# Kernel optimization log

Hardware: AMD Instinct MI355X
Metric: run time of the kernel (lower is better)

The kernel has to match this reference:

```python
import jax, jax.numpy as jnp
import numpy as np

S, B, D = 2048, 2, 1024
NH, DH, DI = 16, 64, 4096


def setup_inputs() -> dict:
    key = jax.random.key(0)
    ks = jax.random.split(key, 12)
    init_qkv = 1.0 / np.sqrt(D)
    init_out = 1.0 / np.sqrt(NH * DH)
    stdm = 1.0 / np.sqrt(D)
    stdi = 1.0 / np.sqrt(DI)

    def u(k, shape, lo, hi):
        return jax.random.uniform(k, shape, jnp.float32, lo, hi)

    inp = {}
    inp["dec_inp"] = jax.random.normal(ks[0], (S, B, D), jnp.float32)
    # causal mask: True = masked (future key j > query i); shape [q, k, batch]
    causal = jnp.triu(jnp.ones((S, S), bool), k=1)
    inp["attn_mask"] = jnp.broadcast_to(causal[:, :, None], (S, S, B))
    inp["query_mean"] = u(ks[1], (NH * DH, D), -init_qkv, init_qkv)
    inp["key_mean"] = u(ks[2], (NH * DH, D), -init_qkv, init_qkv)
    inp["value_mean"] = u(ks[3], (NH * DH, D), -init_qkv, init_qkv)
    inp["query_std"] = u(ks[4], (NH * DH, D), 2 * np.log(init_qkv), np.log(init_qkv))
    inp["key_std"] = u(ks[5], (NH * DH, D), 2 * np.log(init_qkv), np.log(init_qkv))
    inp["value_std"] = u(ks[6], (NH * DH, D), 2 * np.log(init_qkv), np.log(init_qkv))
    inp["output_mean"] = u(ks[7], (D, NH * DH), -init_out, init_out)
    inp["output_std"] = u(ks[8], (D, NH * DH), 2 * np.log(init_out), np.log(init_out))
    inp["ln1_gamma"] = jnp.ones((D,), jnp.float32)
    inp["ln1_beta"] = jnp.zeros((D,), jnp.float32)
    inp["w1_mean"] = u(ks[9], (DI, D), -stdm, stdm)
    inp["w2_mean"] = u(ks[10], (D, DI), -stdi, stdi)
    inp["w1_std"] = u(ks[11], (DI, D), 2 * np.log(stdm), np.log(stdm))
    inp["w2_std"] = u(jax.random.fold_in(key, 99), (D, DI), 2 * np.log(stdi), np.log(stdi))
    inp["ln2_gamma"] = jnp.ones((D,), jnp.float32)
    inp["ln2_beta"] = jnp.zeros((D,), jnp.float32)
    return inp


def _layer_norm(x, g, b, eps=1e-5):
    mu = jnp.mean(x, -1, keepdims=True)
    var = jnp.mean((x - mu) ** 2, -1, keepdims=True)
    return g * (x - mu) * jax.lax.rsqrt(var + eps) + b


def _kl(theta_mean, theta_std):
    return jnp.mean(theta_mean ** 2 - 2.0 * theta_std + jnp.exp(2.0 * theta_std)) / 2.0


def reference(dec_inp, attn_mask, query_mean, key_mean, value_mean, query_std,
              key_std, value_std, output_mean, output_std, ln1_gamma, ln1_beta,
              w1_mean, w2_mean, w1_std, w2_std, ln2_gamma, ln2_beta):
    scale = 1.0 / (DH ** 0.5)
    # QKV projections (eval mode: no Bayesian weight sampling, diffs are 0)
    head_q = jnp.einsum('ibd,hd->ibh', dec_inp, query_mean).reshape(S, B, NH, DH)
    head_k = jnp.einsum('ibd,hd->ibh', dec_inp, key_mean).reshape(S, B, NH, DH)
    head_v = jnp.einsum('ibd,hd->ibh', dec_inp, value_mean).reshape(S, B, NH, DH)
    attn_score = jnp.einsum('ibnd,jbnd->ijbn', head_q, head_k) * scale
    attn_score = jnp.where(attn_mask[:, :, :, None], -jnp.inf, attn_score)
    attn_prob = jax.nn.softmax(attn_score, axis=1)  # softmax over key dim j
    attn_vec = jnp.einsum('ijbn,jbnd->ibnd', attn_prob, head_v).reshape(S, B, NH * DH)
    # NOTE: the original code (bug-faithfully) projects with value_mean, not output_mean
    attn_out = jnp.einsum('ibh,dh->ibd', attn_vec, value_mean)
    h = _layer_norm(dec_inp + attn_out, ln1_gamma, ln1_beta)
    attn_kl = _kl(
        jnp.concatenate([query_mean, key_mean, value_mean, output_mean.T], -1),
        jnp.concatenate([query_std, key_std, value_std, output_std.T], -1))
    # Bayesian positionwise FF (no activation in BayesPositionwiseFF)
    l1 = jnp.einsum('ibd,fd->ibf', h, w1_mean)
    l2 = jnp.einsum('ibf,df->ibd', l1, w2_mean)
    out = _layer_norm(h + l2, ln2_gamma, ln2_beta)
    ff_kl = _kl(jnp.concatenate([w1_mean, w2_mean.T], -1),
                jnp.concatenate([w1_std, w2_std.T], -1))
    return out, attn_kl + ff_kl
```

## Files before the change

### kernel.cpp

```cpp
#include <hip/hip_runtime.h>

#define S_LEN  2048
#define BATCH  2
#define DMODEL 1024
#define NHEADS 16
#define DHEAD  64
#define DFF    4096
#define MROWS  (S_LEN*BATCH)
#define QKVN   3072

typedef __attribute__((ext_vector_type(8))) short bf16x8;
typedef __attribute__((ext_vector_type(4))) float f32x4;
typedef __attribute__((ext_vector_type(4))) short s16x4;

#define NEG_BIG (-3.0e38f)
#define SCALE_LOG2 (0.125f * 1.4426950408889634f)

__device__ __forceinline__ short f2bf(float f){
  unsigned u = __float_as_uint(f);
  u += 0x7fffu + ((u >> 16) & 1u);
  return (short)(u >> 16);
}

__device__ __forceinline__ void gload16(const void* gptr, void* lptr){
  __builtin_amdgcn_global_load_lds(
      (const __attribute__((address_space(1))) unsigned int*)gptr,
      (__attribute__((address_space(3))) unsigned int*)lptr,
      16, 0, 0);
}

__global__ __launch_bounds__(256) void cast_kernel(const float* __restrict__ in,
                                                   short* __restrict__ out, int n){
  int i = (blockIdx.x * 256 + threadIdx.x) * 4;
  if (i >= n) return;
  f32x4 v = *(const f32x4*)(in + i);
  s16x4 o;
  o[0] = f2bf(v[0]); o[1] = f2bf(v[1]); o[2] = f2bf(v[2]); o[3] = f2bf(v[3]);
  *(s16x4*)(out + i) = o;
}

__global__ __launch_bounds__(256) void cast_kl_kernel(const float* __restrict__ mean,
                                                      const float* __restrict__ stdv,
                                                      short* __restrict__ outb,
                                                      int n, double* acc){
  __shared__ double red[4];
  double local = 0.0;
  const int stride = gridDim.x * 1024;
  for (int i = (blockIdx.x * 256 + threadIdx.x) * 4; i < n; i += stride){
    f32x4 m = *(const f32x4*)(mean + i);
    f32x4 sv = *(const f32x4*)(stdv + i);
    if (outb){
      s16x4 o;
      o[0] = f2bf(m[0]); o[1] = f2bf(m[1]); o[2] = f2bf(m[2]); o[3] = f2bf(m[3]);
      *(s16x4*)(outb + i) = o;
    }
    for (int e = 0; e < 4; e++)
      local += (double)(m[e] * m[e]) - 2.0 * (double)sv[e] + (double)expf(2.f * sv[e]);
  }
  for (int msk = 1; msk < 64; msk <<= 1) local += __shfl_xor(local, msk, 64);
  const int t = threadIdx.x;
  if ((t & 63) == 0) red[t >> 6] = local;
  __syncthreads();
  if (t == 0) atomicAdd(acc, red[0] + red[1] + red[2] + red[3]);
}

__global__ void kl_final(const double* acc, float* out){
  out[0] = (float)(acc[0] / 8388608.0 + acc[1] / 16777216.0);
}

template<int BN>
__global__ __launch_bounds__(512) void gemm_bt(const short* __restrict__ A,
                                               const short* __restrict__ Bt,
                                               float* __restrict__ Cf,
                                               short* __restrict__ Cb,
                                               int M, int N, int K, int nbx){
  __shared__ short As[3][128][32];
  __shared__ short Bs[3][BN][32];
  constexpr int NB = BN / 32;
  constexpr int BSTRIDE = BN * 64;
  const int t = threadIdx.x;
  const int lane = t & 63, w = t >> 6;
  const int q8 = (int)gridDim.x >> 3;
  const int sid = ((int)blockIdx.x & 7) * q8 + ((int)blockIdx.x >> 3);
  const int bx = sid % nbx, by = sid / nbx;
  const int m0 = by * 128, n0 = bx * BN;
  const int wm = (w & 3) * 32, wn = (w >> 2) * (BN / 2);
  const int lr = lane & 15, lg = lane >> 4;
  const bool doB = (BN == 128) || (t < 256);

  f32x4 acc[2][NB] = {};

  const short* Ap = A  + (size_t)(m0 + (t >> 2)) * K + (t & 3) * 8;
  const short* Bp = Bt + (size_t)(n0 + ((t & (BN * 4 - 1)) >> 2)) * K + (t & 3) * 8;
  char* ldsA0 = (char*)As + w * 1024;
  char* ldsB0 = (char*)Bs + (w & (NB * 2 - 1)) * 1024;

  const int nk = K / 32;
  for (int p = 0; p < 2; p++){
    gload16(Ap + p * 32, ldsA0 + p * 8192);
    if (doB) gload16(Bp + p * 32, ldsB0 + p * BSTRIDE);
  }

  int bufcur = 0;
  for (int kt = 0; kt < nk; kt++){
    if (kt + 1 < nk){
      if (doB) asm volatile("s_waitcnt vmcnt(2)" ::: "memory");
      else     asm volatile("s_waitcnt vmcnt(1)" ::: "memory");
    } else {
      asm volatile("s_waitcnt vmcnt(0)" ::: "memory");
    }
    __builtin_amdgcn_s_barrier();
    asm volatile("" ::: "memory");

    if (kt + 2 < nk){
      int bnx = bufcur >= 1 ? bufcur - 1 : bufcur + 2;
      gload16(Ap + (kt + 2) * 32, ldsA0 + bnx * 8192);
      if (doB) gload16(Bp + (kt + 2) * 32, ldsB0 + bnx * BSTRIDE);
    }

    bf16x8 a0 = *(const bf16x8*)&As[bufcur][wm      + lr][lg * 8];
    bf16x8 a1 = *(const bf16x8*)&As[bufcur][wm + 16 + lr][lg * 8];
    bf16x8 bfr[NB];
    for (int ni = 0; ni < NB; ni++)
      bfr[ni] = *(const bf16x8*)&Bs[bufcur][wn + ni * 16 + lr][lg * 8];
    __builtin_amdgcn_s_setprio(1);
    for (int ni = 0; ni < NB; ni++){
      acc[0][ni] = __builtin_amdgcn_mfma_f32_16x16x32_bf16(a0, bfr[ni], acc[0][ni], 0, 0, 0);
      acc[1][ni] = __builtin_amdgcn_mfma_f32_16x16x32_bf16(a1, bfr[ni], acc[1][ni], 0, 0, 0);
    }
    __builtin_amdgcn_s_setprio(0);
    bufcur = bufcur < 2 ? bufcur + 1 : 0;
  }

  for (int mi = 0; mi < 2; mi++){
    for (int ni = 0; ni < NB; ni++){
      int row = m0 + wm + mi * 16 + lg * 4;
      int col = n0 + wn + ni * 16 + lr;
      for (int r = 0; r < 4; r++){
        float v = acc[mi][ni][r];
        if (Cf) Cf[(size_t)(row + r) * N + col] = v;
        if (Cb) Cb[(size_t)(row + r) * N + col] = f2bf(v);
      }
    }
  }
}

__global__ __launch_bounds__(256) void attn_kernel(const short* __restrict__ QKV,
                                                   short* __restrict__ AV){
  __shared__ short Ks[64][64];
  __shared__ short Vst[64][64];
  __shared__ short Pt[4][16][64];
  const int t = threadIdx.x, lane = t & 63, w = t >> 6;
  const int hb = blockIdx.y;
  const int b = hb >> 4, n = hb & 15;
  const int lr = lane & 15, lg = lane >> 4;

  for (int half = 0; half < 2; half++){
    const int qt = half ? (31 - (int)blockIdx.x) : (int)blockIdx.x;
    const int q0w = qt * 64 + w * 16;

    bf16x8 aq[2];
    {
      const short* qp = QKV + ((size_t)(q0w + lr) * BATCH + b) * QKVN + n * DHEAD + lg * 8;
      aq[0] = *(const bf16x8*)(qp);
      aq[1] = *(const bf16x8*)(qp + 32);
    }

    f32x4 acc[4] = {};
    float m_run = NEG_BIG, l_run = 0.f;

    for (int jt = 0; jt <= qt; jt++){
      const int j0 = jt * 64;
      __syncthreads();
      {
        int j = t >> 2, u0 = (t & 3) * 2;
        const short* kp = QKV + ((size_t)(j0 + j) * BATCH + b) * QKVN + DMODEL + n * DHEAD + u0 * 8;
        *(bf16x8*)&Ks[j][(u0 ^ (j & 7)) * 8]       = *(const bf16x8*)(kp);
        *(bf16x8*)&Ks[j][((u0 + 1) ^ (j & 7)) * 8] = *(const bf16x8*)(kp + 8);
        int jv = t & 63, dq = (t >> 6) * 16;
        const short* vp = QKV + ((size_t)(j0 + jv) * BATCH + b) * QKVN + 2 * DMODEL + n * DHEAD + dq;
        bf16x8 v0 = *(const bf16x8*)(vp);
        bf16x8 v1 = *(const bf16x8*)(vp + 8);
        int uj = jv >> 3, jl = jv & 7;
        for (int e = 0; e < 8; e++){
          int sc = (((uj ^ e) << 3) | jl);
          Vst[dq + e][sc]     = v0[e];
          Vst[dq + 8 + e][sc] = v1[e];
        }
      }
      __syncthreads();

      f32x4 s[4];
      __builtin_amdgcn_s_setprio(1);
      for (int nf = 0; nf < 4; nf++){
        f32x4 z = {};
        for (int kk = 0; kk < 2; kk++){
          bf16x8 bk = *(const bf16x8*)&Ks[nf * 16 + lr][((kk * 4 + lg) ^ (lr & 7)) * 8];
          z = __builtin_amdgcn_mfma_f32_16x16x32_bf16(bk, aq[kk], z, 0, 0, 0);
        }
        s[nf] = z;
      }
      __builtin_amdgcn_s_setprio(0);

      if (jt == qt){
        int qg = q0w + lr;
        for (int nf = 0; nf < 4; nf++)
          for (int r = 0; r < 4; r++)
            if (j0 + nf * 16 + lg * 4 + r > qg) s[nf][r] = NEG_BIG;
      }

      float mx = NEG_BIG;
      for (int nf = 0; nf < 4; nf++){
        float a0 = fmaxf(s[nf][0], s[nf][1]);
        float a1 = fmaxf(s[nf][2], s[nf][3]);
        mx = fmaxf(mx, fmaxf(a0, a1));
      }
      mx = fmaxf(mx, __shfl_xor(mx, 16, 64));
      mx = fmaxf(mx, __shfl_xor(mx, 32, 64));
      float mxs = mx * SCALE_LOG2;

      if (__any(mxs > m_run + 8.f)){
        float mn = fmaxf(m_run, mxs);
        float corr = __builtin_exp2f(m_run - mn);
        m_run = mn;
        l_run *= corr;
        float cb[4];
        for (int r = 0; r < 4; r++) cb[r] = __shfl(corr, lg * 4 + r, 64);
        for (int df = 0; df < 4; df++)
          for (int r = 0; r < 4; r++) acc[df][r] *= cb[r];
      }

      float rs = 0.f;
      for (int nf = 0; nf < 4; nf++)
        for (int r = 0; r < 4; r++){
          float p = __builtin_exp2f(fmaf(s[nf][r], SCALE_LOG2, -m_run));
          s[nf][r] = p;
          rs += p;
        }
      rs += __shfl_xor(rs, 16, 64);
      rs += __shfl_xor(rs, 32, 64);
      l_run += rs;

      char* prow = (char*)&Pt[w][lr][0];
      for (int nf = 0; nf < 4; nf++){
        unsigned u0 = __float_as_uint(s[nf][0]);
        unsigned u1 = __float_as_uint(s[nf][1]);
        unsigned u2 = __float_as_uint(s[nf][2]);
        unsigned u3 = __float_as_uint(s[nf][3]);
        uint2 val;
        val.x = (u0 >> 16) | (u1 & 0xffff0000u);
        val.y = (u2 >> 16) | (u3 & 0xffff0000u);
        int off = ((((nf * 2) + (lg >> 1)) ^ (lr & 7)) << 4) + ((lg & 1) << 3);
        *(uint2*)(prow + off) = val;
      }

      __builtin_amdgcn_s_setprio(1);
      for (int kk = 0; kk < 2; kk++){
        bf16x8 pa = *(const bf16x8*)(prow + ((((kk * 4) + lg) ^ (lr & 7)) << 4));
        for (int df = 0; df < 4; df++){
          bf16x8 bv = *(const bf16x8*)&Vst[df * 16 + lr][((kk * 4 + lg) ^ (lr & 7)) * 8];
          acc[df] = __builtin_amdgcn_mfma_f32_16x16x32_bf16(pa, bv, acc[df], 0, 0, 0);
        }
      }
      __builtin_amdgcn_s_setprio(0);
    }

    float lb[4];
    for (int r = 0; r < 4; r++) lb[r] = __shfl(l_run, lg * 4 + r, 64);
    for (int df = 0; df < 4; df++){
      for (int r = 0; r < 4; r++){
        int i_glob = q0w + lg * 4 + r;
        AV[((size_t)i_glob * BATCH + b) * DMODEL + n * DHEAD + df * 16 + lr] =
            f2bf(acc[df][r] / lb[r]);
      }
    }
    __syncthreads();
  }
}

__global__ __launch_bounds__(256) void ln_kernel(const float* __restrict__ xa,
                                                 const float* __restrict__ xb,
                                                 const float* __restrict__ gamma,
                                                 const float* __restrict__ beta,
                                                 float* __restrict__ outF,
                                                 short* __restrict__ outB){
  __shared__ float red[4];
  const int row = blockIdx.x, t = threadIdx.x;
  const size_t base = (size_t)row * DMODEL + t * 4;
  f32x4 a  = *(const f32x4*)(xa + base);
  f32x4 bb = *(const f32x4*)(xb + base);
  f32x4 x;
  for (int e = 0; e < 4; e++) x[e] = a[e] + bb[e];
  float sum = x[0] + x[1] + x[2] + x[3];
  for (int m = 1; m < 64; m <<= 1) sum += __shfl_xor(sum, m, 64);
  if ((t & 63) == 0) red[t >> 6] = sum;
  __syncthreads();
  float mu = (red[0] + red[1] + red[2] + red[3]) * (1.f / DMODEL);
  float sq = 0.f;
  for (int e = 0; e < 4; e++){ float d = x[e] - mu; sq += d * d; }
  for (int m = 1; m < 64; m <<= 1) sq += __shfl_xor(sq, m, 64);
  __syncthreads();
  if ((t & 63) == 0) red[t >> 6] = sq;
  __syncthreads();
  float var = (red[0] + red[1] + red[2] + red[3]) * (1.f / DMODEL);
  float rstd = rsqrtf(var + 1e-5f);
  f32x4 g  = *(const f32x4*)(gamma + t * 4);
  f32x4 be = *(const f32x4*)(beta + t * 4);
  for (int e = 0; e < 4; e++){
    float y = g[e] * (x[e] - mu) * rstd + be[e];
    if (outF) outF[base + e] = y;
    if (outB) outB[base + e] = f2bf(y);
  }
}

extern "C" void kernel_launch(void* const* d_in, const int* in_sizes, int n_in,
                              void* d_out, int out_size, void* d_ws, size_t ws_size,
                              hipStream_t stream){
  (void)in_sizes; (void)n_in; (void)out_size; (void)ws_size;
  const float* dec = (const float*)d_in[0];
  const float* qm  = (const float*)d_in[2];
  const float* km  = (const float*)d_in[3];
  const float* vm  = (const float*)d_in[4];
  const float* qs  = (const float*)d_in[5];
  const float* ks  = (const float*)d_in[6];
  const float* vs  = (const float*)d_in[7];
  const float* om  = (const float*)d_in[8];
  const float* os_ = (const float*)d_in[9];
  const float* g1  = (const float*)d_in[10];
  const float* b1  = (const float*)d_in[11];
  const float* w1m = (const float*)d_in[12];
  const float* w2m = (const float*)d_in[13];
  const float* w1s = (const float*)d_in[14];
  const float* w2s = (const float*)d_in[15];
  const float* g2  = (const float*)d_in[16];
  const float* b2  = (const float*)d_in[17];
  float* out = (float*)d_out;

  char* ws = (char*)d_ws;
  size_t off = 0;
  auto alloc = [&](size_t bytes) -> char* {
    char* p = ws + off;
    off += (bytes + 255) & ~(size_t)255;
    return p;
  };
  short* Xb   = (short*)alloc((size_t)MROWS * DMODEL * 2);
  short* Wqkv = (short*)alloc((size_t)QKVN * DMODEL * 2);
  short* W1   = (short*)alloc((size_t)DFF * DMODEL * 2);
  short* W2   = (short*)alloc((size_t)DMODEL * DFF * 2);
  short* Wv   = Wqkv + (size_t)2 * DMODEL * DMODEL;
  short* QKVb = (short*)alloc((size_t)MROWS * QKVN * 2);
  short* AVb  = (short*)alloc((size_t)MROWS * DMODEL * 2);
  float* tmpF = (float*)alloc((size_t)MROWS * DMODEL * 4);
  float* hF   = (float*)alloc((size_t)MROWS * DMODEL * 4);
  double* acc = (double*)alloc(256);
  short* L1 = QKVb;

  hipMemsetAsync(acc, 0, 16, stream);

  cast_kernel<<<MROWS * DMODEL / 1024, 256, 0, stream>>>(dec, Xb, MROWS * DMODEL);
  cast_kl_kernel<<<1024, 256, 0, stream>>>(qm, qs, Wqkv, DMODEL * DMODEL, acc);
  cast_kl_kernel<<<1024, 256, 0, stream>>>(km, ks, Wqkv + (size_t)DMODEL * DMODEL, DMODEL * DMODEL, acc);
  cast_kl_kernel<<<1024, 256, 0, stream>>>(vm, vs, Wqkv + (size_t)2 * DMODEL * DMODEL, DMODEL * DMODEL, acc);
  cast_kl_kernel<<<1024, 256, 0, stream>>>(om, os_, nullptr, DMODEL * DMODEL, acc);
  cast_kl_kernel<<<1024, 256, 0, stream>>>(w1m, w1s, W1, DFF * DMODEL, acc + 1);
  cast_kl_kernel<<<1024, 256, 0, stream>>>(w2m, w2s, W2, DMODEL * DFF, acc + 1);

  gemm_bt<128><<<(QKVN / 128) * (MROWS / 128), 512, 0, stream>>>(Xb, Wqkv, nullptr, QKVb, MROWS, QKVN, DMODEL, QKVN / 128);

  attn_kernel<<<dim3(16, BATCH * NHEADS), 256, 0, stream>>>(QKVb, AVb);

  gemm_bt<64><<<(DMODEL / 64) * (MROWS / 128), 512, 0, stream>>>(AVb, Wv, tmpF, nullptr, MROWS, DMODEL, DMODEL, DMODEL / 64);

  ln_kernel<<<MROWS, 256, 0, stream>>>(dec, tmpF, g1, b1, hF, Xb);

  gemm_bt<128><<<(DFF / 128) * (MROWS / 128), 512, 0, stream>>>(Xb, W1, nullptr, L1, MROWS, DFF, DMODEL, DFF / 128);
  gemm_bt<64><<<(DMODEL / 64) * (MROWS / 128), 512, 0, stream>>>(L1, W2, tmpF, nullptr, MROWS, DMODEL, DFF, DMODEL / 64);

  ln_kernel<<<MROWS, 256, 0, stream>>>(hF, tmpF, g2, b2, out, nullptr);

  kl_final<<<1, 1, 0, stream>>>(acc, out + (size_t)MROWS * DMODEL);
}
```

Measured before the change: 535.3 us.

## Batch KL casts, bf16 GEMM outputs, remap GEMM tiles, simplify softmax rescale

The six cast/KL launches become two multi-tensor launches, and the final KL reduction is folded into the last layernorm kernel, so there are fewer launches. The two N=1024 GEMMs now write bf16 instead of fp32, which halves their output traffic and the layernorm input reads, at some cost in precision. The GEMM block-to-tile mapping is changed so each XCD gets a contiguous band of columns, aimed at better L2 reuse. In attention, the lazy threshold-based max rescale is replaced by an unconditional rescale on every tile, with the scale applied before the max.

Result: faster. 479.0 us (-10.5%).

```diff
diff --git a/kernel.cpp b/kernel.cpp
--- a/kernel.cpp
+++ b/kernel.cpp
@@ -21,6 +21,9 @@
   u += 0x7fffu + ((u >> 16) & 1u);
   return (short)(u >> 16);
 }
+__device__ __forceinline__ float bf2f(short s){
+  return __uint_as_float(((unsigned)(unsigned short)s) << 16);
+}
 
 __device__ __forceinline__ void gload16(const void* gptr, void* lptr){
   __builtin_amdgcn_global_load_lds(
@@ -39,20 +42,30 @@
   *(s16x4*)(out + i) = o;
 }
 
-__global__ __launch_bounds__(256) void cast_kl_kernel(const float* __restrict__ mean,
-                                                      const float* __restrict__ stdv,
-                                                      short* __restrict__ outb,
-                                                      int n, double* acc){
+__global__ __launch_bounds__(256) void cast_kl_multi(
+    const float* __restrict__ m0, const float* __restrict__ s0, short* o0,
+    const float* __restrict__ m1, const float* __restrict__ s1, short* o1,
+    const float* __restrict__ m2, const float* __restrict__ s2, short* o2,
+    const float* __restrict__ m3, const float* __restrict__ s3, short* o3,
+    int n, double* acc){
   __shared__ double red[4];
+  const float* mm; const float* ss; short* oo;
+  switch (blockIdx.y){
+    case 0: mm = m0; ss = s0; oo = o0; break;
+    case 1: mm = m1; ss = s1; oo = o1; break;
+    case 2: mm = m2; ss = s2; oo = o2; break;
+    default: mm = m3; ss = s3; oo = o3; break;
+  }
+  if (!mm) return;
   double local = 0.0;
   const int stride = gridDim.x * 1024;
   for (int i = (blockIdx.x * 256 + threadIdx.x) * 4; i < n; i += stride){
-    f32x4 m = *(const f32x4*)(mean + i);
-    f32x4 sv = *(const f32x4*)(stdv + i);
-    if (outb){
+    f32x4 m = *(const f32x4*)(mm + i);
+    f32x4 sv = *(const f32x4*)(ss + i);
+    if (oo){
       s16x4 o;
       o[0] = f2bf(m[0]); o[1] = f2bf(m[1]); o[2] = f2bf(m[2]); o[3] = f2bf(m[3]);
-      *(s16x4*)(outb + i) = o;
+      *(s16x4*)(oo + i) = o;
     }
     for (int e = 0; e < 4; e++)
       local += (double)(m[e] * m[e]) - 2.0 * (double)sv[e] + (double)expf(2.f * sv[e]);
@@ -62,10 +75,6 @@
   if ((t & 63) == 0) red[t >> 6] = local;
   __syncthreads();
   if (t == 0) atomicAdd(acc, red[0] + red[1] + red[2] + red[3]);
-}
-
-__global__ void kl_final(const double* acc, float* out){
-  out[0] = (float)(acc[0] / 8388608.0 + acc[1] / 16777216.0);
 }
 
 template<int BN>
@@ -80,9 +89,11 @@
   constexpr int BSTRIDE = BN * 64;
   const int t = threadIdx.x;
   const int lane = t & 63, w = t >> 6;
-  const int q8 = (int)gridDim.x >> 3;
-  const int sid = ((int)blockIdx.x & 7) * q8 + ((int)blockIdx.x >> 3);
-  const int bx = sid % nbx, by = sid / nbx;
+  const int bpx = nbx >> 3;
+  const int xcd = (int)blockIdx.x & 7;
+  const int jj  = (int)blockIdx.x >> 3;
+  const int bx = xcd * bpx + (jj % bpx);
+  const int by = jj / bpx;
   const int m0 = by * 128, n0 = bx * BN;
   const int wm = (w & 3) * 32, wn = (w >> 2) * (BN / 2);
   const int lr = lane & 15, lg = lane >> 4;
@@ -202,6 +213,9 @@
       }
       __builtin_amdgcn_s_setprio(0);
 
+      for (int nf = 0; nf < 4; nf++)
+        for (int r = 0; r < 4; r++) s[nf][r] *= SCALE_LOG2;
+
       if (jt == qt){
         int qg = q0w + lr;
         for (int nf = 0; nf < 4; nf++)
@@ -217,29 +231,20 @@
       }
       mx = fmaxf(mx, __shfl_xor(mx, 16, 64));
       mx = fmaxf(mx, __shfl_xor(mx, 32, 64));
-      float mxs = mx * SCALE_LOG2;
-
-      if (__any(mxs > m_run + 8.f)){
-        float mn = fmaxf(m_run, mxs);
-        float corr = __builtin_exp2f(m_run - mn);
-        m_run = mn;
-        l_run *= corr;
-        float cb[4];
-        for (int r = 0; r < 4; r++) cb[r] = __shfl(corr, lg * 4 + r, 64);
-        for (int df = 0; df < 4; df++)
-          for (int r = 0; r < 4; r++) acc[df][r] *= cb[r];
-      }
+      float mn = fmaxf(m_run, mx);
+      float corr = __builtin_exp2f(m_run - mn);
+      m_run = mn;
 
       float rs = 0.f;
       for (int nf = 0; nf < 4; nf++)
         for (int r = 0; r < 4; r++){
-          float p = __builtin_exp2f(fmaf(s[nf][r], SCALE_LOG2, -m_run));
+          float p = __builtin_exp2f(s[nf][r] - mn);
           s[nf][r] = p;
           rs += p;
         }
       rs += __shfl_xor(rs, 16, 64);
       rs += __shfl_xor(rs, 32, 64);
-      l_run += rs;
+      l_run = l_run * corr + rs;
 
       char* prow = (char*)&Pt[w][lr][0];
       for (int nf = 0; nf < 4; nf++){
@@ -254,6 +259,11 @@
         *(uint2*)(prow + off) = val;
       }
 
+      float cb[4];
+      for (int r = 0; r < 4; r++) cb[r] = __shfl(corr, lg * 4 + r, 64);
+      for (int df = 0; df < 4; df++)
+        for (int r = 0; r < 4; r++) acc[df][r] *= cb[r];
+
       __builtin_amdgcn_s_setprio(1);
       for (int kk = 0; kk < 2; kk++){
         bf16x8 pa = *(const bf16x8*)(prow + ((((kk * 4) + lg) ^ (lr & 7)) << 4));
@@ -279,18 +289,20 @@
 }
 
 __global__ __launch_bounds__(256) void ln_kernel(const float* __restrict__ xa,
-                                                 const float* __restrict__ xb,
+                                                 const short* __restrict__ xbB,
                                                  const float* __restrict__ gamma,
                                                  const float* __restrict__ beta,
                                                  float* __restrict__ outF,
-                                                 short* __restrict__ outB){
+                                                 short* __restrict__ outB,
+                                                 const double* __restrict__ klacc,
+                                                 float* __restrict__ klout){
   __shared__ float red[4];
   const int row = blockIdx.x, t = threadIdx.x;
   const size_t base = (size_t)row * DMODEL + t * 4;
   f32x4 a  = *(const f32x4*)(xa + base);
-  f32x4 bb = *(const f32x4*)(xb + base);
+  s16x4 bb = *(const s16x4*)(xbB + base);
   f32x4 x;
-  for (int e = 0; e < 4; e++) x[e] = a[e] + bb[e];
+  for (int e = 0; e < 4; e++) x[e] = a[e] + bf2f(bb[e]);
   float sum = x[0] + x[1] + x[2] + x[3];
   for (int m = 1; m < 64; m <<= 1) sum += __shfl_xor(sum, m, 64);
   if ((t & 63) == 0) red[t >> 6] = sum;
@@ -311,6 +323,8 @@
     if (outF) outF[base + e] = y;
     if (outB) outB[base + e] = f2bf(y);
   }
+  if (klout && row == 0 && t == 0)
+    klout[0] = (float)(klacc[0] / 8388608.0 + klacc[1] / 16777216.0);
 }
 
 extern "C" void kernel_launch(void* const* d_in, const int* in_sizes, int n_in,
@@ -350,7 +364,7 @@
   short* Wv   = Wqkv + (size_t)2 * DMODEL * DMODEL;
   short* QKVb = (short*)alloc((size_t)MROWS * QKVN * 2);
   short* AVb  = (short*)alloc((size_t)MROWS * DMODEL * 2);
-  float* tmpF = (float*)alloc((size_t)MROWS * DMODEL * 4);
+  short* tmpB = (short*)alloc((size_t)MROWS * DMODEL * 2);
   float* hF   = (float*)alloc((size_t)MROWS * DMODEL * 4);
   double* acc = (double*)alloc(256);
   short* L1 = QKVb;
@@ -358,25 +372,29 @@
   hipMemsetAsync(acc, 0, 16, stream);
 
   cast_kernel<<<MROWS * DMODEL / 1024, 256, 0, stream>>>(dec, Xb, MROWS * DMODEL);
-  cast_kl_kernel<<<1024, 256, 0, stream>>>(qm, qs, Wqkv, DMODEL * DMODEL, acc);
-  cast_kl_kernel<<<1024, 256, 0, stream>>>(km, ks, Wqkv + (size_t)DMODEL * DMODEL, DMODEL * DMODEL, acc);
-  cast_kl_kernel<<<1024, 256, 0, stream>>>(vm, vs, Wqkv + (size_t)2 * DMODEL * DMODEL, DMODEL * DMODEL, acc);
-  cast_kl_kernel<<<1024, 256, 0, stream>>>(om, os_, nullptr, DMODEL * DMODEL, acc);
-  cast_kl_kernel<<<1024, 256, 0, stream>>>(w1m, w1s, W1, DFF * DMODEL, acc + 1);
-  cast_kl_kernel<<<1024, 256, 0, stream>>>(w2m, w2s, W2, DMODEL * DFF, acc + 1);
+  cast_kl_multi<<<dim3(256, 4), 256, 0, stream>>>(
+      qm, qs, Wqkv,
+      km, ks, Wqkv + (size_t)DMODEL * DMODEL,
+      vm, vs, Wqkv + (size_t)2 * DMODEL * DMODEL,
+      om, os_, nullptr,
+      DMODEL * DMODEL, acc);
+  cast_kl_multi<<<dim3(512, 2), 256, 0, stream>>>(
+      w1m, w1s, W1,
+      w2m, w2s, W2,
+      nullptr, nullptr, nullptr,
+      nullptr, nullptr, nullptr,
+      DFF * DMODEL, acc + 1);
 
   gemm_bt<128><<<(QKVN / 128) * (MROWS / 128), 512, 0, stream>>>(Xb, Wqkv, nullptr, QKVb, MROWS, QKVN, DMODEL, QKVN / 128);
 
   attn_kernel<<<dim3(16, BATCH * NHEADS), 256, 0, stream>>>(QKVb, AVb);
 
-  gemm_bt<64><<<(DMODEL / 64) * (MROWS / 128), 512, 0, stream>>>(AVb, Wv, tmpF, nullptr, MROWS, DMODEL, DMODEL, DMODEL / 64);
-
-  ln_kernel<<<MROWS, 256, 0, stream>>>(dec, tmpF, g1, b1, hF, Xb);
+  gemm_bt<64><<<(DMODEL / 64) * (MROWS / 128), 512, 0, stream>>>(AVb, Wv, nullptr, tmpB, MROWS, DMODEL, DMODEL, DMODEL / 64);
+
+  ln_kernel<<<MROWS, 256, 0, stream>>>(dec, tmpB, g1, b1, hF, Xb, nullptr, nullptr);
 
   gemm_bt<128><<<(DFF / 128) * (MROWS / 128), 512, 0, stream>>>(Xb, W1, nullptr, L1, MROWS, DFF, DMODEL, DFF / 128);
-  gemm_bt<64><<<(DMODEL / 64) * (MROWS / 128), 512, 0, stream>>>(L1, W2, tmpF, nullptr, MROWS, DMODEL, DFF, DMODEL / 64);
-
-  ln_kernel<<<MROWS, 256, 0, stream>>>(hF, tmpF, g2, b2, out, nullptr);
-
-  kl_final<<<1, 1, 0, stream>>>(acc, out + (size_t)MROWS * DMODEL);
-}
+  gemm_bt<64><<<(DMODEL / 64) * (MROWS / 128), 512, 0, stream>>>(L1, W2, nullptr, tmpB, MROWS, DMODEL, DFF, DMODEL / 64);
+
+  ln_kernel<<<MROWS, 256, 0, stream>>>(hF, tmpB, g2, b2, out, nullptr, acc, out + (size_t)MROWS * DMODEL);
+}
```
